# Performance work log

Measured on AMD Instinct MI355X. Metric: run time of the kernel, lower is better.

Reference implementation:

```python
import jax, jax.numpy as jnp
import numpy as np

B, IH, IW = 16, 32, 32
N = IH * IW
HEADS, DIM_HEAD = 8, 64
INNER = HEADS * DIM_HEAD  # 512
INP, OUP = 512, 512
SCALE = DIM_HEAD ** -0.5


def _relative_index():
    # replicate torch.meshgrid (ij) -> coords [2, N]
    yy, xx = np.meshgrid(np.arange(IH), np.arange(IW), indexing='ij')
    coords = np.stack([yy.reshape(-1), xx.reshape(-1)])  # [2, N]
    rel = coords[:, :, None] - coords[:, None, :]        # [2, N, N]
    rel[0] += IH - 1
    rel[1] += IW - 1
    rel[0] *= 2 * IW - 1
    return jnp.asarray(rel.sum(0).reshape(-1), dtype=jnp.int32)  # [N*N]


def setup_inputs() -> dict:
    key = jax.random.key(0)
    k1, k2, k3, k4, k5 = jax.random.split(key, 5)
    x = jax.random.normal(k1, (B, N, INP), dtype=jnp.float32)
    W_qkv = jax.random.normal(k2, (INP, 3 * INNER), dtype=jnp.float32) * (INP ** -0.5)
    # table is initialized to zeros in the module; use small randn so bias path is exercised
    rel_table = jax.random.normal(k3, ((2 * IH - 1) * (2 * IW - 1), HEADS), dtype=jnp.float32) * 0.02
    W_out = jax.random.normal(k4, (INNER, OUP), dtype=jnp.float32) * (INNER ** -0.5)
    b_out = jax.random.normal(k5, (OUP,), dtype=jnp.float32) * 0.02
    return {
        'x': x,
        'W_qkv': W_qkv,
        'rel_table': rel_table,
        'W_out': W_out,
        'b_out': b_out,
        'rel_index': _relative_index(),
    }


def reference(x, W_qkv, rel_table, W_out, b_out, rel_index):
    b, n, _ = x.shape
    qkv = x @ W_qkv                                            # [b, n, 3*inner]
    q, k, v = jnp.split(qkv, 3, axis=-1)
    def to_heads(t):
        return t.reshape(b, n, HEADS, DIM_HEAD).transpose(0, 2, 1, 3)  # [b, h, n, d]
    q, k, v = to_heads(q), to_heads(k), to_heads(v)
    dots = jnp.einsum('bhnd,bhmd->bhnm', q, k) * SCALE         # [b, h, n, n]
    bias = rel_table[rel_index].reshape(n, n, HEADS).transpose(2, 0, 1)[None]  # [1, h, n, n]
    attn = jax.nn.softmax(dots + bias, axis=-1)
    out = jnp.einsum('bhnm,bhmd->bhnd', attn, v)               # [b, h, n, d]
    out = out.transpose(0, 2, 1, 3).reshape(b, n, INNER)       # [b, n, inner]
    return out @ W_out + b_out
```

## Files before the change

### kernel.cpp

```cpp
#include <hip/hip_runtime.h>
#include <math.h>

#define BATCH 16
#define NTOK 1024
#define HEADS 8
#define DHEAD 64
#define INNER 512
#define QKV_COLS 1536
#define SCALE_L2E 0.1803368801111244f
#define LOG2E 1.4426950408889634f

#if __has_builtin(__builtin_amdgcn_exp2f)
#define EXP2F(x) __builtin_amdgcn_exp2f(x)
#else
#define EXP2F(x) __expf((x) * 0.6931471805599453f)
#endif

typedef _Float16 f16x8 __attribute__((ext_vector_type(8)));
typedef _Float16 f16x4 __attribute__((ext_vector_type(4)));
typedef float f32x4 __attribute__((ext_vector_type(4)));

#define MFMA32(a, b, c) __builtin_amdgcn_mfma_f32_16x16x32_f16(a, b, c, 0, 0, 0)

__device__ __forceinline__ void glds16(const void* g, void* l) {
    __builtin_amdgcn_global_load_lds(
        (const __attribute__((address_space(1))) unsigned int*)g,
        (__attribute__((address_space(3))) unsigned int*)l, 16, 0, 0);
}

#define XV (BATCH * NTOK * INNER / 4)
#define WQ (INNER * QKV_COLS)
#define WO (INNER * INNER)

__global__ __launch_bounds__(256)
void convert_inputs(const float* __restrict__ x, const float* __restrict__ Wq,
                    const float* __restrict__ Wo, _Float16* __restrict__ x_h,
                    _Float16* __restrict__ Wq_t, _Float16* __restrict__ Wo_t) {
    int idx = blockIdx.x * 256 + threadIdx.x;
    if (idx < XV) {
        float4 v = ((const float4*)x)[idx];
        f16x4 h;
        h[0] = (_Float16)v.x; h[1] = (_Float16)v.y;
        h[2] = (_Float16)v.z; h[3] = (_Float16)v.w;
        *(f16x4*)(x_h + (size_t)idx * 4) = h;
    } else if (idx < XV + WQ) {
        int i = idx - XV;
        int n = i >> 9, k = i & 511;
        Wq_t[i] = (_Float16)Wq[k * QKV_COLS + n];
    } else if (idx < XV + WQ + WO) {
        int i = idx - XV - WQ;
        int n = i >> 9, k = i & 511;
        Wo_t[i] = (_Float16)Wo[k * INNER + n];
    }
}

template<int MODE>
__global__ __launch_bounds__(256, 3)
void gemm_f16(const _Float16* __restrict__ A, const _Float16* __restrict__ Bt,
              const float* __restrict__ bias, void* __restrict__ Cout,
              _Float16* __restrict__ vtg, int M, int N, int K) {
    __shared__ _Float16 As[3][128 * 32];
    __shared__ _Float16 Bs[3][128 * 32];

    const int t    = threadIdx.x;
    const int l    = t & 63;
    const int w    = t >> 6;
    const int wm   = w >> 1;
    const int wn   = w & 1;
    const int quad = l >> 4;
    const int lrow = l & 15;

    const int nwg = gridDim.x * gridDim.y;
    int bid = blockIdx.x + gridDim.x * blockIdx.y;
    bid = (bid & 7) * (nwg >> 3) + (bid >> 3);
    const size_t row0 = (size_t)(bid / gridDim.x) * 128;
    const size_t col0 = (size_t)(bid % gridDim.x) * 128;

    const int srow = t >> 2;
    const int sch  = t & 3;

    f32x4 acc[4][4] = {};
    const int NSTEP = K >> 5;

    auto stage = [&](int kk, int bufi) {
#pragma unroll
        for (int p = 0; p < 2; ++p) {
            const int r  = p * 64 + srow;
            const int gc = (sch ^ ((r >> 1) & 3)) * 8;
            glds16(A  + (row0 + r) * K + kk * 32 + gc, (char*)As[bufi] + p * 4096 + t * 16);
            glds16(Bt + (col0 + r) * K + kk * 32 + gc, (char*)Bs[bufi] + p * 4096 + t * 16);
        }
    };

    stage(0, 0);
    stage(1, 1);

    int buf = 0, pre = 2;
    for (int kk = 0; kk < NSTEP; ++kk) {
        if (kk + 1 < NSTEP) asm volatile("s_waitcnt vmcnt(4)" ::: "memory");
        else                asm volatile("s_waitcnt vmcnt(0)" ::: "memory");
        __builtin_amdgcn_s_barrier();
        __builtin_amdgcn_sched_barrier(0);
        if (kk + 2 < NSTEP) stage(kk + 2, pre);

        f16x8 af[4], bf[4];
#pragma unroll
        for (int i = 0; i < 4; ++i) {
            const int r = wm * 64 + i * 16 + lrow;
            af[i] = *(const f16x8*)(As[buf] + r * 32 + ((quad ^ ((r >> 1) & 3)) * 8));
        }
#pragma unroll
        for (int j = 0; j < 4; ++j) {
            const int r = wn * 64 + j * 16 + lrow;
            bf[j] = *(const f16x8*)(Bs[buf] + r * 32 + ((quad ^ ((r >> 1) & 3)) * 8));
        }
#pragma unroll
        for (int i = 0; i < 4; ++i)
#pragma unroll
            for (int j = 0; j < 4; ++j)
                acc[i][j] = MFMA32(bf[j], af[i], acc[i][j]);

        buf = (buf == 2) ? 0 : buf + 1;
        pre = (pre == 2) ? 0 : pre + 1;
    }

    const bool isV = (MODE == 2) && (col0 >= 2 * INNER);
#pragma unroll
    for (int i = 0; i < 4; ++i) {
        const size_t m = row0 + wm * 64 + i * 16 + lrow;
#pragma unroll
        for (int j = 0; j < 4; ++j) {
            const size_t c = col0 + wn * 64 + j * 16 + quad * 4;
            f32x4 v = acc[i][j];
            if (MODE == 0) {
                float4 bv = *(const float4*)(bias + c);
                v[0] += bv.x; v[1] += bv.y; v[2] += bv.z; v[3] += bv.w;
                *(f32x4*)((float*)Cout + m * N + c) = v;
            } else if (!isV) {
                f16x4 hv;
                hv[0] = (_Float16)v[0]; hv[1] = (_Float16)v[1];
                hv[2] = (_Float16)v[2]; hv[3] = (_Float16)v[3];
                *(f16x4*)((_Float16*)Cout + m * N + c) = hv;
            } else {
                const int cv = (int)(c - 2 * INNER);
                const int hh = cv >> 6, db = cv & 63;
                const size_t vb = (((size_t)(m >> 10) * HEADS + hh) * 64 + db) * NTOK
                                  + (m & (NTOK - 1));
#pragma unroll
                for (int reg = 0; reg < 4; ++reg)
                    vtg[vb + (size_t)reg * NTOK] = (_Float16)v[reg];
            }
        }
    }
}

__global__ __launch_bounds__(512, 4)
void attn_f16_v7(const _Float16* __restrict__ qkv, const _Float16* __restrict__ vt,
                 const float* __restrict__ rel_table, _Float16* __restrict__ out) {
    __shared__ _Float16 Ks[2][64 * 64];
    __shared__ _Float16 Vs[2][64 * 64];
    __shared__ float biasS[3969];

    const int t    = threadIdx.x;
    const int l    = t & 63;
    const int w    = t >> 6;
    const int quad = l >> 4;
    const int lrow = l & 15;
    const int h    = blockIdx.y;
    const int bb   = blockIdx.z;
    const int qr0  = blockIdx.x * 256 + w * 32;

    for (int idx = t; idx < 3969; idx += 512)
        biasS[idx] = rel_table[idx * HEADS + h] * LOG2E;

    const size_t tokbase = (size_t)bb * NTOK;

    f16x8 aq[2][2];
#pragma unroll
    for (int mt = 0; mt < 2; ++mt)
#pragma unroll
        for (int ksi = 0; ksi < 2; ++ksi)
            aq[mt][ksi] = *(const f16x8*)(qkv + (tokbase + qr0 + mt * 16 + lrow) * QKV_COLS
                                          + h * DHEAD + ksi * 32 + quad * 8);

    f32x4 O[2][4] = {};
    float l0 = 0.f, l1 = 0.f;

    const int iy = qr0 >> 5;
    const int krow_base = 8 * (lrow >> 2) + (lrow & 3);
    const int fKl = (lrow & 3) + 4 * ((lrow >> 2) & 1);

    const int kr  = t >> 3;
    const int ksl = t & 7;
    const int fKr = (kr & 3) + 4 * ((kr >> 3) & 1);
    const _Float16* kbase = qkv + tokbase * QKV_COLS + INNER + h * DHEAD;
    const _Float16* vbase = vt + ((size_t)(bb * HEADS + h) * 64) * NTOK;

    auto stage = [&](int jt, int bufi) {
        const int j0s = jt * 64;
        glds16(kbase + (size_t)(j0s + kr) * QKV_COLS + (ksl ^ fKr) * 8, (char*)Ks[bufi] + t * 16);
        glds16(vbase + (size_t)kr * NTOK + j0s + (ksl ^ (kr & 7)) * 8,  (char*)Vs[bufi] + t * 16);
    };

    stage(0, 0);

    for (int jt = 0; jt < 16; ++jt) {
        const int buf = jt & 1;
        __syncthreads();
        if (jt < 15) stage(jt + 1, buf ^ 1);

#pragma unroll
        for (int jn0 = 0; jn0 < 2; ++jn0) {
            f16x8 pb0, pb1;
#pragma unroll
            for (int s = 0; s < 2; ++s) {
                const int krow = jn0 * 32 + krow_base + 4 * s;
                f32x4 S0 = {}, S1 = {};
                __builtin_amdgcn_s_setprio(1);
#pragma unroll
                for (int ksi = 0; ksi < 2; ++ksi) {
                    f16x8 bk = *(const f16x8*)(Ks[buf] + krow * 64
                                               + (((ksi * 4 + quad) ^ fKl) * 8));
                    S0 = MFMA32(bk, aq[0][ksi], S0);
                    S1 = MFMA32(bk, aq[1][ksi], S1);
                }
                __builtin_amdgcn_s_setprio(0);
                const int base = (iy - (jt * 2 + jn0) + 31) * 63 + 31 + lrow
                                 - 8 * quad - 4 * s;
                {
                    float p0 = EXP2F(fmaf(S0[0], SCALE_L2E, biasS[base - 0]));
                    float p1 = EXP2F(fmaf(S0[1], SCALE_L2E, biasS[base - 1]));
                    float p2 = EXP2F(fmaf(S0[2], SCALE_L2E, biasS[base - 2]));
                    float p3 = EXP2F(fmaf(S0[3], SCALE_L2E, biasS[base - 3]));
                    l0 += (p0 + p1) + (p2 + p3);
                    pb0[s * 4 + 0] = (_Float16)p0; pb0[s * 4 + 1] = (_Float16)p1;
                    pb0[s * 4 + 2] = (_Float16)p2; pb0[s * 4 + 3] = (_Float16)p3;
                }
                {
                    const int b1 = base + 16;
                    float p0 = EXP2F(fmaf(S1[0], SCALE_L2E, biasS[b1 - 0]));
                    float p1 = EXP2F(fmaf(S1[1], SCALE_L2E, biasS[b1 - 1]));
                    float p2 = EXP2F(fmaf(S1[2], SCALE_L2E, biasS[b1 - 2]));
                    float p3 = EXP2F(fmaf(S1[3], SCALE_L2E, biasS[b1 - 3]));
                    l1 += (p0 + p1) + (p2 + p3);
                    pb1[s * 4 + 0] = (_Float16)p0; pb1[s * 4 + 1] = (_Float16)p1;
                    pb1[s * 4 + 2] = (_Float16)p2; pb1[s * 4 + 3] = (_Float16)p3;
                }
            }

            __builtin_amdgcn_s_setprio(1);
#pragma unroll
            for (int dn = 0; dn < 4; ++dn) {
                const int d = dn * 16 + lrow;
                f16x8 av = *(const f16x8*)(Vs[buf] + d * 64
                              + (((jn0 * 4 + quad) ^ (d & 7)) * 8));
                O[0][dn] = MFMA32(av, pb0, O[0][dn]);
                O[1][dn] = MFMA32(av, pb1, O[1][dn]);
            }
            __builtin_amdgcn_s_setprio(0);
        }
    }

#pragma unroll
    for (int mt = 0; mt < 2; ++mt) {
        float s = mt ? l1 : l0;
        s += __shfl_xor(s, 16);
        s += __shfl_xor(s, 32);
        const float inv = 1.f / s;
        const size_t orow = (tokbase + qr0 + mt * 16 + lrow) * INNER + h * DHEAD;
#pragma unroll
        for (int dn = 0; dn < 4; ++dn) {
            const f32x4 o = O[mt][dn];
            f16x4 ov;
            ov[0] = (_Float16)(o[0] * inv); ov[1] = (_Float16)(o[1] * inv);
            ov[2] = (_Float16)(o[2] * inv); ov[3] = (_Float16)(o[3] * inv);
            *(f16x4*)(out + orow + dn * 16 + quad * 4) = ov;
        }
    }
}

extern "C" void kernel_launch(void* const* d_in, const int* in_sizes, int n_in,
                              void* d_out, int out_size, void* d_ws, size_t ws_size,
                              hipStream_t stream) {
    const float* x         = (const float*)d_in[0];
    const float* W_qkv     = (const float*)d_in[1];
    const float* rel_table = (const float*)d_in[2];
    const float* W_out     = (const float*)d_in[3];
    const float* b_out     = (const float*)d_in[4];

    _Float16* x_h   = (_Float16*)d_ws;
    _Float16* Wq_t  = x_h + (size_t)BATCH * NTOK * INNER;
    _Float16* Wo_t  = Wq_t + (size_t)INNER * QKV_COLS;
    _Float16* qkv_h = Wo_t + (size_t)INNER * INNER;
    _Float16* att_h = qkv_h + (size_t)BATCH * NTOK * QKV_COLS;
    _Float16* vt_g  = att_h + (size_t)BATCH * NTOK * INNER;

    const int M = BATCH * NTOK;

    convert_inputs<<<(XV + WQ + WO + 255) / 256, 256, 0, stream>>>(
        x, W_qkv, W_out, x_h, Wq_t, Wo_t);

    gemm_f16<2><<<dim3(QKV_COLS / 128, M / 128), 256, 0, stream>>>(
        x_h, Wq_t, nullptr, qkv_h, vt_g, M, QKV_COLS, INNER);

    attn_f16_v7<<<dim3(NTOK / 256, HEADS, BATCH), 512, 0, stream>>>(
        qkv_h, vt_g, rel_table, att_h);

    gemm_f16<0><<<dim3(INNER / 128, M / 128), 256, 0, stream>>>(
        att_h, Wo_t, b_out, d_out, nullptr, M, INNER, INNER);
}
```

Measured before the change: 205.6 us.

## Triple-buffer attention K/V staging and tile the weight transpose-convert

The attention kernel moves from double to triple buffering of K/V tiles in LDS, prefetching two tiles ahead. It synchronises with explicit vmcnt waits and a raw s_barrier instead of __syncthreads, to hide global-to-LDS load latency better. The weight conversion kernel now transposes W_qkv and W_out in 64x64 tiles with vectorized loads and stores instead of one scalar strided read per element. The extra LDS buffer raises shared memory per block, which may reduce occupancy, and the hand-written waitcnt logic is a correctness risk if the counts do not match the outstanding loads.

```diff
diff --git a/kernel.cpp b/kernel.cpp
--- a/kernel.cpp
+++ b/kernel.cpp
@@ -29,28 +29,42 @@
 }
 
 #define XV (BATCH * NTOK * INNER / 4)
-#define WQ (INNER * QKV_COLS)
-#define WO (INNER * INNER)
+#define XB (XV / 256)
+#define WQTILES 192
+#define WOTILES 64
 
 __global__ __launch_bounds__(256)
 void convert_inputs(const float* __restrict__ x, const float* __restrict__ Wq,
                     const float* __restrict__ Wo, _Float16* __restrict__ x_h,
                     _Float16* __restrict__ Wq_t, _Float16* __restrict__ Wo_t) {
-    int idx = blockIdx.x * 256 + threadIdx.x;
-    if (idx < XV) {
+    const int b = blockIdx.x, t = threadIdx.x;
+    if (b < XB) {
+        const int idx = b * 256 + t;
         float4 v = ((const float4*)x)[idx];
         f16x4 h;
         h[0] = (_Float16)v.x; h[1] = (_Float16)v.y;
         h[2] = (_Float16)v.z; h[3] = (_Float16)v.w;
         *(f16x4*)(x_h + (size_t)idx * 4) = h;
-    } else if (idx < XV + WQ) {
-        int i = idx - XV;
-        int n = i >> 9, k = i & 511;
-        Wq_t[i] = (_Float16)Wq[k * QKV_COLS + n];
-    } else if (idx < XV + WQ + WO) {
-        int i = idx - XV - WQ;
-        int n = i >> 9, k = i & 511;
-        Wo_t[i] = (_Float16)Wo[k * INNER + n];
+        return;
+    }
+    const bool isQ = (b < XB + WQTILES);
+    const int b2  = isQ ? (b - XB) : (b - XB - WQTILES);
+    const int ntl = isQ ? 24 : 8;
+    const int ldw = isQ ? QKV_COLS : INNER;
+    const float*   W  = isQ ? Wq   : Wo;
+    _Float16*      Wt = isQ ? Wq_t : Wo_t;
+    const int k0 = (b2 / ntl) * 64, n0 = (b2 % ntl) * 64;
+    const int kk = k0 + (t >> 4) * 4, nn = n0 + (t & 15) * 4;
+    f32x4 v0 = *(const f32x4*)(W + (size_t)(kk + 0) * ldw + nn);
+    f32x4 v1 = *(const f32x4*)(W + (size_t)(kk + 1) * ldw + nn);
+    f32x4 v2 = *(const f32x4*)(W + (size_t)(kk + 2) * ldw + nn);
+    f32x4 v3 = *(const f32x4*)(W + (size_t)(kk + 3) * ldw + nn);
+#pragma unroll
+    for (int f = 0; f < 4; ++f) {
+        f16x4 h;
+        h[0] = (_Float16)v0[f]; h[1] = (_Float16)v1[f];
+        h[2] = (_Float16)v2[f]; h[3] = (_Float16)v3[f];
+        *(f16x4*)(Wt + (size_t)(nn + f) * INNER + kk) = h;
     }
 }
 
@@ -155,10 +169,10 @@
 }
 
 __global__ __launch_bounds__(512, 4)
-void attn_f16_v7(const _Float16* __restrict__ qkv, const _Float16* __restrict__ vt,
+void attn_f16_v8(const _Float16* __restrict__ qkv, const _Float16* __restrict__ vt,
                  const float* __restrict__ rel_table, _Float16* __restrict__ out) {
-    __shared__ _Float16 Ks[2][64 * 64];
-    __shared__ _Float16 Vs[2][64 * 64];
+    __shared__ _Float16 Ks[3][64 * 64];
+    __shared__ _Float16 Vs[3][64 * 64];
     __shared__ float biasS[3969];
 
     const int t    = threadIdx.x;
@@ -203,11 +217,16 @@
     };
 
     stage(0, 0);
-
+    stage(1, 1);
+    asm volatile("s_waitcnt lgkmcnt(0)" ::: "memory");
+
+    int buf = 0, pre = 2;
     for (int jt = 0; jt < 16; ++jt) {
-        const int buf = jt & 1;
-        __syncthreads();
-        if (jt < 15) stage(jt + 1, buf ^ 1);
+        if (jt < 15) asm volatile("s_waitcnt vmcnt(2)" ::: "memory");
+        else         asm volatile("s_waitcnt vmcnt(0)" ::: "memory");
+        __builtin_amdgcn_s_barrier();
+        __builtin_amdgcn_sched_barrier(0);
+        if (jt + 2 < 16) stage(jt + 2, pre);
 
 #pragma unroll
         for (int jn0 = 0; jn0 < 2; ++jn0) {
@@ -259,6 +278,9 @@
             }
             __builtin_amdgcn_s_setprio(0);
         }
+
+        buf = (buf == 2) ? 0 : buf + 1;
+        pre = (pre == 2) ? 0 : pre + 1;
     }
 
 #pragma unroll
@@ -297,13 +319,13 @@
 
     const int M = BATCH * NTOK;
 
-    convert_inputs<<<(XV + WQ + WO + 255) / 256, 256, 0, stream>>>(
+    convert_inputs<<<XB + WQTILES + WOTILES, 256, 0, stream>>>(
         x, W_qkv, W_out, x_h, Wq_t, Wo_t);
 
     gemm_f16<2><<<dim3(QKV_COLS / 128, M / 128), 256, 0, stream>>>(
         x_h, Wq_t, nullptr, qkv_h, vt_g, M, QKV_COLS, INNER);
 
-    attn_f16_v7<<<dim3(NTOK / 256, HEADS, BATCH), 512, 0, stream>>>(
+    attn_f16_v8<<<dim3(NTOK / 256, HEADS, BATCH), 512, 0, stream>>>(
         qkv_h, vt_g, rel_table, att_h);
 
     gemm_f16<0><<<dim3(INNER / 128, M / 128), 256, 0, stream>>>(
```

Result: no change. 205.9 us (+0.1%).
